# Optimization experiments

Hardware: AMD Instinct MI355X
Metric: run time of the kernel (lower is better)

## Reference

```python
import jax, jax.numpy as jnp
import numpy as np

N_NODES = 50000


def _add_self_loops(edge_index, n):
    loops = jnp.arange(n, dtype=edge_index.dtype)
    src = jnp.concatenate([edge_index[0], loops])
    dst = jnp.concatenate([edge_index[1], loops])
    return src, dst


def _gcn_norm(src, dst, n):
    # symmetric normalization deg^-1/2 (degrees include self-loops), as in PyG GCNConv
    ones = jnp.ones_like(dst, dtype=jnp.float32)
    deg = jax.ops.segment_sum(ones, dst, num_segments=n)
    dinv = jnp.where(deg > 0, jax.lax.rsqrt(deg), 0.0)
    return dinv[src] * dinv[dst]


def _gcn_conv(x, W, b, src, dst, norm, n):
    h = x @ W                                  # [N, d_out] dense transform first (d_out <= d_in)
    msg = h[src] * norm[:, None]               # gather + per-edge scale
    out = jax.ops.segment_sum(msg, dst, num_segments=n)  # scatter-add aggregation
    return out + b


def setup_inputs() -> dict:
    key = jax.random.key(0)
    ks = jax.random.split(key, 5)
    n, e = N_NODES, 1_600_000
    x = jax.random.normal(ks[0], (n, 512), dtype=jnp.float32)
    edge_index = jax.random.randint(ks[1], (2, e), 0, n, dtype=jnp.int64)
    def glorot(k, fi, fo):
        s = jnp.sqrt(6.0 / (fi + fo)).astype(jnp.float32)
        return jax.random.uniform(k, (fi, fo), jnp.float32, -s, s)
    return {
        "x": x,
        "edge_index": edge_index,
        "W0": glorot(ks[2], 512, 256), "b0": jnp.zeros((256,), jnp.float32),
        "W1": glorot(ks[3], 256, 256), "b1": jnp.zeros((256,), jnp.float32),
        "W2": glorot(ks[4], 256, 128), "b2": jnp.zeros((128,), jnp.float32),
    }


def reference(x, edge_index, W0, b0, W1, b1, W2, b2):
    n = x.shape[0]
    src, dst = _add_self_loops(edge_index, n)
    norm = _gcn_norm(src, dst, n)
    h = jax.nn.relu(_gcn_conv(x, W0, b0, src, dst, norm, n))
    h = jax.nn.relu(_gcn_conv(h, W1, b1, src, dst, norm, n))
    z = _gcn_conv(h, W2, b2, src, dst, norm, n)
    return z
```

## Files before the change

### kernel.cpp

```cpp
#include <hip/hip_runtime.h>
#include <hip/hip_bf16.h>
#include <type_traits>

#define NN 50000
#define CNT_S 16

typedef __attribute__((ext_vector_type(8))) short bf16x8;
typedef __attribute__((ext_vector_type(4))) float f32x4;
typedef unsigned int u32;

__device__ __forceinline__ ushort f2bf(float f) {
    unsigned u = __builtin_bit_cast(unsigned, f);
    unsigned r = (u + 0x7fffu + ((u >> 16) & 1u)) >> 16;
    return (ushort)r;
}
__device__ __forceinline__ float bflo(unsigned v) { return __builtin_bit_cast(float, v << 16); }
__device__ __forceinline__ float bfhi(unsigned v) { return __builtin_bit_cast(float, v & 0xffff0000u); }

__device__ __forceinline__ void gld16(const void* g, void* l) {
    __builtin_amdgcn_global_load_lds((const __attribute__((address_space(1))) u32*)g,
                                     (__attribute__((address_space(3))) u32*)l, 16, 0, 0);
}

__global__ void k_initw(int* cnt, int ncnt, const unsigned int* ei, int npairs, int* flag,
                        const float* __restrict__ W0, ushort* __restrict__ WT0,
                        const float* __restrict__ W1, ushort* __restrict__ WT1,
                        const float* __restrict__ W2, ushort* __restrict__ WT2) {
    int id = blockIdx.x * 256 + threadIdx.x;
    if (id < ncnt) cnt[id] = 0;
    if (blockIdx.x == 0) {
        __shared__ int any_nz;
        if (threadIdx.x == 0) any_nz = 0;
        __syncthreads();
        for (int p = threadIdx.x; p < npairs; p += blockDim.x) {
            if (ei[2 * p + 1] != 0u) atomicOr(&any_nz, 1);
        }
        __syncthreads();
        if (threadIdx.x == 0) *flag = (any_nz == 0) ? 1 : 0;
    }
    const float* W; ushort* WT; int K, N, loc;
    if (id < 131072)      { W = W0; WT = WT0; K = 512; N = 256; loc = id; }
    else if (id < 196608) { W = W1; WT = WT1; K = 256; N = 256; loc = id - 131072; }
    else if (id < 229376) { W = W2; WT = WT2; K = 256; N = 128; loc = id - 196608; }
    else return;
    int nn = loc / K, k = loc - nn * K;
    WT[loc] = f2bf(W[(long long)k * N + nn]);
}

__device__ __forceinline__ int load_idx(const void* ei, long long pos, int is64) {
    return is64 ? (int)(((const long long*)ei)[pos]) : ((const int*)ei)[pos];
}

__global__ void k_count(const void* ei, long long E, const int* flag,
                        int* cnt, int* __restrict__ ord) {
    long long e = (long long)blockIdx.x * blockDim.x + threadIdx.x;
    if (e < E) {
        int dst = load_idx(ei, E + e, *flag);
        ord[e] = atomicAdd(&cnt[(long long)dst * CNT_S], 1);
    }
}

__global__ void k_scan(const int* __restrict__ cnt, int* __restrict__ offs,
                       float* __restrict__ dinv, int n) {
    __shared__ int wsum[16];
    __shared__ int carry_s;
    int t = (int)threadIdx.x;
    int lane = t & 63, w = t >> 6;
    if (t == 0) carry_s = 0;
    __syncthreads();
    for (int base = 0; base < n; base += 1024) {
        int i = base + t;
        int v = (i < n) ? cnt[(long long)i * CNT_S] : 0;
        int pv = (v + 7) & ~7;
        int x = pv;
#pragma unroll
        for (int off = 1; off < 64; off <<= 1) {
            int y = __shfl_up(x, off);
            if (lane >= off) x += y;
        }
        if (lane == 63) wsum[w] = x;
        __syncthreads();
        if (w == 0) {
            int pvv = (lane < 16) ? wsum[lane] : 0;
#pragma unroll
            for (int off = 1; off < 16; off <<= 1) {
                int py = __shfl_up(pvv, off);
                if (lane >= off) pvv += py;
            }
            if (lane < 16) wsum[lane] = pvv;
        }
        __syncthreads();
        int wbase = (w > 0) ? wsum[w - 1] : 0;
        int incl = x + wbase;
        int excl = incl - pv;
        int carry = carry_s;
        if (i < n) {
            offs[i] = carry + excl;
            dinv[i] = rsqrtf((float)(v + 1));
        }
        __syncthreads();
        if (t == 1023) carry_s = carry + incl;
        __syncthreads();
    }
    if (threadIdx.x == 0) offs[n] = carry_s;
}

#define KE 8
__global__ void k_bucket(const void* ei, long long E, const int* __restrict__ flag,
                         const float* __restrict__ dinv, const int* __restrict__ offs,
                         const int* __restrict__ ord, int2* __restrict__ epk,
                         const int* __restrict__ cnt, int n, int nchunk_e, int pn) {
    int p = blockIdx.x & 7;
    int c = blockIdx.x >> 3;
    int lo = p * pn;
    int hi = lo + pn; if (hi > n) hi = n;
    if (c < nchunk_e) {
        int is64 = *flag;
        long long base = (long long)c * (256 * KE) + threadIdx.x;
#pragma unroll
        for (int k = 0; k < KE; ++k) {
            long long e = base + k * 256;
            if (e < E) {
                int dst = load_idx(ei, E + e, is64);
                if (dst >= lo && dst < hi) {
                    int src = load_idx(ei, e, is64);
                    int pos = offs[dst] + ord[e];
                    epk[pos] = make_int2(src, __builtin_bit_cast(int, dinv[src] * dinv[dst]));
                }
            }
        }
    } else {
        int i = lo + (c - nchunk_e) * 256 + (int)threadIdx.x;
        if (i < hi) {
            int b = offs[i] + cnt[(long long)i * CNT_S], en = offs[i + 1];
            for (int j = b; j < en; ++j) epk[j] = make_int2(0, 0);
        }
    }
}

__global__ void k_x2bf(const float* __restrict__ x, ushort* __restrict__ xbf, long long n8) {
    long long id = (long long)blockIdx.x * blockDim.x + threadIdx.x;
    if (id < n8) {
        const float* src = x + id * 8;
        float4 f0 = *(const float4*)src;
        float4 f1 = *(const float4*)(src + 4);
        ushort tmp[8] = {f2bf(f0.x), f2bf(f0.y), f2bf(f0.z), f2bf(f0.w),
                         f2bf(f1.x), f2bf(f1.y), f2bf(f1.z), f2bf(f1.w)};
        *(uint4*)&xbf[id * 8] = *(uint4*)tmp;
    }
}

#define LOFF(r, s) (((r) * 8 + ((s) ^ ((r) & 7))) * 8)

template <typename TA>
__global__ __launch_bounds__(256) void k_gemm_mfma(const TA* __restrict__ A,
                                                   const ushort* __restrict__ WT,
                                                   ushort* __restrict__ C,
                                                   int M, int N, int K) {
    __shared__ ushort As[8192];
    __shared__ ushort Bs[8192];
    int t = threadIdx.x;
    int lane = t & 63;
    int w = t >> 6;
    int wr = (w >> 1) * 64, wc = (w & 1) * 64;
    int m0 = blockIdx.y * 128, n0 = blockIdx.x * 128;

    f32x4 acc[4][4] = {};

    for (int k0 = 0; k0 < K; k0 += 64) {
#pragma unroll
        for (int j = 0; j < 4; ++j) {
            int id = (w * 4 + j) * 64 + lane;
            int r = id >> 3, sp = id & 7;
            int s = sp ^ (r & 7);
            gld16(WT + (long long)(n0 + r) * K + k0 + s * 8, &Bs[(r * 8 + sp) * 8]);
        }
        if constexpr (std::is_same<TA, float>::value) {
#pragma unroll
            for (int j = 0; j < 4; ++j) {
                int id = t + j * 256;
                int r = id >> 3, s = id & 7;
                int grow = m0 + r;
                if (grow < M) {
                    const float* src = A + (long long)grow * K + k0 + s * 8;
                    float4 f0 = *(const float4*)src;
                    float4 f1 = *(const float4*)(src + 4);
                    ushort tmp[8] = {f2bf(f0.x), f2bf(f0.y), f2bf(f0.z), f2bf(f0.w),
                                     f2bf(f1.x), f2bf(f1.y), f2bf(f1.z), f2bf(f1.w)};
                    *(uint4*)&As[LOFF(r, s)] = *(uint4*)tmp;
                }
            }
        } else {
#pragma unroll
            for (int j = 0; j < 4; ++j) {
                int rbase = (w * 4 + j) * 8;
                if (m0 + rbase < M) {
                    int id = rbase * 8 + lane;
                    int r = id >> 3, sp = id & 7;
                    int s = sp ^ (r & 7);
                    gld16((const ushort*)A + (long long)(m0 + r) * K + k0 + s * 8,
                          &As[(r * 8 + sp) * 8]);
                }
            }
        }
        __syncthreads();
#pragma unroll
        for (int kk = 0; kk < 2; ++kk) {
            int ks = kk * 4 + (lane >> 4);
            bf16x8 a[4], b[4];
#pragma unroll
            for (int m = 0; m < 4; ++m)
                a[m] = *(bf16x8*)&As[LOFF(wr + m * 16 + (lane & 15), ks)];
#pragma unroll
            for (int nn = 0; nn < 4; ++nn)
                b[nn] = *(bf16x8*)&Bs[LOFF(wc + nn * 16 + (lane & 15), ks)];
#pragma unroll
            for (int m = 0; m < 4; ++m)
#pragma unroll
                for (int nn = 0; nn < 4; ++nn)
                    acc[m][nn] = __builtin_amdgcn_mfma_f32_16x16x32_bf16(a[m], b[nn], acc[m][nn], 0, 0, 0);
        }
        __syncthreads();
    }
#pragma unroll
    for (int m = 0; m < 4; ++m) {
#pragma unroll
        for (int i = 0; i < 4; ++i) {
            int row = m0 + wr + m * 16 + (lane >> 4) * 4 + i;
            if (row < M) {
#pragma unroll
                for (int nn = 0; nn < 4; ++nn) {
                    int col = n0 + wc + nn * 16 + (lane & 15);
                    C[(long long)row * N + col] = f2bf(acc[m][nn][i]);
                }
            }
        }
    }
}

template <int DT, bool RELU, bool OUTF32>
__global__ __launch_bounds__(128) void k_aggs(const ushort* __restrict__ h,
                                              const int* __restrict__ offs,
                                              const int2* __restrict__ epk,
                                              const float* __restrict__ dinv,
                                              const float* __restrict__ bias,
                                              void* __restrict__ outp, int n, int foff) {
    int node = __builtin_amdgcn_readfirstlane((int)(blockIdx.x * 2 + (threadIdx.x >> 6)));
    if (node >= n) return;
    int t = (int)threadIdx.x & 63;
    float di = dinv[node];
    float dii = di * di;

    unsigned v0 = *(const unsigned*)&h[(long long)node * DT + foff + t * 2];
    float2 bs = *(const float2*)&bias[foff + t * 2];
    float a0 = bs.x + dii * bflo(v0);
    float a1 = bs.y + dii * bfhi(v0);

    int s = offs[node], e = offs[node + 1];

    for (int j = s; j < e; j += 8) {
        int2 p[8];
#pragma unroll
        for (int u = 0; u < 8; ++u) p[u] = epk[j + u];
        unsigned v[8];
#pragma unroll
        for (int u = 0; u < 8; ++u)
            v[u] = *(const unsigned*)&h[(long long)p[u].x * DT + foff + t * 2];
#pragma unroll
        for (int u = 0; u < 8; ++u) {
            float wgt = __builtin_bit_cast(float, p[u].y);
            a0 += wgt * bflo(v[u]);
            a1 += wgt * bfhi(v[u]);
        }
    }

    if (RELU) { a0 = fmaxf(a0, 0.f); a1 = fmaxf(a1, 0.f); }
    long long oidx = ((long long)node * DT + foff) / 2 + t;
    if constexpr (OUTF32) {
        ((float2*)outp)[oidx] = make_float2(a0, a1);
    } else {
        unsigned pk = (unsigned)f2bf(a0) | ((unsigned)f2bf(a1) << 16);
        ((unsigned*)outp)[oidx] = pk;
    }
}

extern "C" void kernel_launch(void* const* d_in, const int* in_sizes, int n_in,
                              void* d_out, int out_size, void* d_ws, size_t ws_size,
                              hipStream_t stream) {
    const float* x  = (const float*)d_in[0];
    const void*  ei = d_in[1];
    const float* W0 = (const float*)d_in[2];
    const float* b0 = (const float*)d_in[3];
    const float* W1 = (const float*)d_in[4];
    const float* b1 = (const float*)d_in[5];
    const float* W2 = (const float*)d_in[6];
    const float* b2 = (const float*)d_in[7];
    float* out = (float*)d_out;

    const int n = NN;
    const long long E = (long long)in_sizes[1] / 2;
    const int ncnt = n * CNT_S;

    char* ws = (char*)d_ws;
    int*    cnt  = (int*)(ws);
    int*    offs = (int*)(ws + 3400 * 1024);
    float*  dinv = (float*)(ws + 3700 * 1024);
    int*    flag = (int*)(ws + 3960 * 1024);
    int2*   epk  = (int2*)(ws + 4ll * 1024 * 1024);
    ushort* WT0  = (ushort*)(ws + 20ll * 1024 * 1024);
    ushort* WT1  = (ushort*)(ws + 20ll * 1024 * 1024 + 512 * 1024);
    ushort* WT2  = (ushort*)(ws + 20ll * 1024 * 1024 + 768 * 1024);
    ushort* hA   = (ushort*)(ws + 21ll * 1024 * 1024);
    ushort* hB   = (ushort*)(ws + 47ll * 1024 * 1024);
    ushort* xbf  = (ushort*)(ws + 73ll * 1024 * 1024);
    int*    ord  = (int*)hA;
    const size_t need_xbf = 73ll * 1024 * 1024 + 51200000ll;
    const bool have_xbf = (ws_size >= need_xbf);

    {
        int nb = (ncnt + 255) / 256;
        k_initw<<<nb, 256, 0, stream>>>(cnt, ncnt, (const unsigned int*)ei, 4096, flag,
                                        W0, WT0, W1, WT1, W2, WT2);
    }

    k_count<<<(int)((E + 255) / 256), 256, 0, stream>>>(ei, E, flag, cnt, ord);
    k_scan<<<1, 1024, 0, stream>>>(cnt, offs, dinv, n);
    {
        int nchunk_e = (int)((E + 256 * KE - 1) / (256 * KE));
        int pn = (n + 7) / 8;
        int nchunk_pad = (pn + 255) / 256;
        k_bucket<<<8 * (nchunk_e + nchunk_pad), 256, 0, stream>>>(
            ei, E, flag, dinv, offs, ord, epk, cnt, n, nchunk_e, pn);
    }
    if (have_xbf) {
        long long n8 = (long long)n * 512 / 8;
        k_x2bf<<<(int)((n8 + 255) / 256), 256, 0, stream>>>(x, xbf, n8);
    }

    int mt = (n + 127) / 128;
    int nb2 = (n + 1) / 2;

    if (have_xbf) {
        k_gemm_mfma<ushort><<<dim3(2, mt), 256, 0, stream>>>(xbf, WT0, hA, n, 256, 512);
    } else {
        k_gemm_mfma<float><<<dim3(2, mt), 256, 0, stream>>>(x, WT0, hA, n, 256, 512);
    }
    k_aggs<256, true, false><<<nb2, 128, 0, stream>>>(hA, offs, epk, dinv, b0, hB, n, 0);
    k_aggs<256, true, false><<<nb2, 128, 0, stream>>>(hA, offs, epk, dinv, b0, hB, n, 128);

    k_gemm_mfma<ushort><<<dim3(2, mt), 256, 0, stream>>>(hB, WT1, hA, n, 256, 256);
    k_aggs<256, true, false><<<nb2, 128, 0, stream>>>(hA, offs, epk, dinv, b1, hB, n, 0);
    k_aggs<256, true, false><<<nb2, 128, 0, stream>>>(hA, offs, epk, dinv, b1, hB, n, 128);

    k_gemm_mfma<ushort><<<dim3(1, mt), 256, 0, stream>>>(hB, WT2, hA, n, 128, 256);
    k_aggs<128, false, true><<<nb2, 128, 0, stream>>>(hA, offs, epk, dinv, b2, out, n, 0);
}
```

Before: 515.2 us.

## Replace single-block degree scan with three-phase multi-block scan

The exclusive prefix scan over node degrees used to run in one 1024-thread block that looped serially over all nodes. It is now split into three kernels: per-block reduction (which also writes dinv), a single-wavefront scan of the block sums, and a per-block local scan that adds the block base. This spreads the scan across about 49 blocks instead of one, at the cost of two extra kernel launches and reading the counts twice.

```diff
diff --git a/kernel.cpp b/kernel.cpp
--- a/kernel.cpp
+++ b/kernel.cpp
@@ -60,49 +60,70 @@
     }
 }
 
-__global__ void k_scan(const int* __restrict__ cnt, int* __restrict__ offs,
-                       float* __restrict__ dinv, int n) {
+__global__ __launch_bounds__(1024) void k_scan_a(const int* __restrict__ cnt,
+                                                 int* __restrict__ bsum,
+                                                 float* __restrict__ dinv, int n) {
     __shared__ int wsum[16];
-    __shared__ int carry_s;
-    int t = (int)threadIdx.x;
-    int lane = t & 63, w = t >> 6;
-    if (t == 0) carry_s = 0;
+    int i = blockIdx.x * 1024 + threadIdx.x;
+    int lane = (int)threadIdx.x & 63, w = (int)threadIdx.x >> 6;
+    int v = (i < n) ? cnt[(long long)i * CNT_S] : 0;
+    int pv = (v + 7) & ~7;
+    if (i < n) dinv[i] = rsqrtf((float)(v + 1));
+    int s = pv;
+#pragma unroll
+    for (int off = 1; off < 64; off <<= 1) s += __shfl_xor(s, off);
+    if (lane == 0) wsum[w] = s;
     __syncthreads();
-    for (int base = 0; base < n; base += 1024) {
-        int i = base + t;
-        int v = (i < n) ? cnt[(long long)i * CNT_S] : 0;
-        int pv = (v + 7) & ~7;
-        int x = pv;
-#pragma unroll
-        for (int off = 1; off < 64; off <<= 1) {
-            int y = __shfl_up(x, off);
-            if (lane >= off) x += y;
-        }
-        if (lane == 63) wsum[w] = x;
-        __syncthreads();
-        if (w == 0) {
-            int pvv = (lane < 16) ? wsum[lane] : 0;
-#pragma unroll
-            for (int off = 1; off < 16; off <<= 1) {
-                int py = __shfl_up(pvv, off);
-                if (lane >= off) pvv += py;
-            }
-            if (lane < 16) wsum[lane] = pvv;
-        }
-        __syncthreads();
-        int wbase = (w > 0) ? wsum[w - 1] : 0;
-        int incl = x + wbase;
-        int excl = incl - pv;
-        int carry = carry_s;
-        if (i < n) {
-            offs[i] = carry + excl;
-            dinv[i] = rsqrtf((float)(v + 1));
-        }
-        __syncthreads();
-        if (t == 1023) carry_s = carry + incl;
-        __syncthreads();
-    }
-    if (threadIdx.x == 0) offs[n] = carry_s;
+    if (threadIdx.x == 0) {
+        int t = 0;
+#pragma unroll
+        for (int k = 0; k < 16; ++k) t += wsum[k];
+        bsum[blockIdx.x] = t;
+    }
+}
+
+__global__ void k_scan_b(const int* __restrict__ bsum, int* __restrict__ bbase,
+                         int* __restrict__ offs_n, int nb) {
+    int lane = (int)threadIdx.x;
+    int v = (lane < nb) ? bsum[lane] : 0;
+    int x = v;
+#pragma unroll
+    for (int off = 1; off < 64; off <<= 1) {
+        int y = __shfl_up(x, off);
+        if (lane >= off) x += y;
+    }
+    if (lane < nb) bbase[lane] = x - v;
+    if (lane == nb - 1) *offs_n = x;
+}
+
+__global__ __launch_bounds__(1024) void k_scan_c(const int* __restrict__ cnt,
+                                                 const int* __restrict__ bbase,
+                                                 int* __restrict__ offs, int n) {
+    __shared__ int wsum[16];
+    int i = blockIdx.x * 1024 + threadIdx.x;
+    int lane = (int)threadIdx.x & 63, w = (int)threadIdx.x >> 6;
+    int v = (i < n) ? cnt[(long long)i * CNT_S] : 0;
+    int pv = (v + 7) & ~7;
+    int x = pv;
+#pragma unroll
+    for (int off = 1; off < 64; off <<= 1) {
+        int y = __shfl_up(x, off);
+        if (lane >= off) x += y;
+    }
+    if (lane == 63) wsum[w] = x;
+    __syncthreads();
+    if (w == 0) {
+        int pvv = (lane < 16) ? wsum[lane] : 0;
+#pragma unroll
+        for (int off = 1; off < 16; off <<= 1) {
+            int py = __shfl_up(pvv, off);
+            if (lane >= off) pvv += py;
+        }
+        if (lane < 16) wsum[lane] = pvv;
+    }
+    __syncthreads();
+    int wbase = (w > 0) ? wsum[w - 1] : 0;
+    if (i < n) offs[i] = bbase[blockIdx.x] + wbase + x - pv;
 }
 
 #define KE 8
@@ -300,12 +321,15 @@
     const int n = NN;
     const long long E = (long long)in_sizes[1] / 2;
     const int ncnt = n * CNT_S;
+    const int nbscan = (n + 1023) / 1024;
 
     char* ws = (char*)d_ws;
     int*    cnt  = (int*)(ws);
     int*    offs = (int*)(ws + 3400 * 1024);
     float*  dinv = (float*)(ws + 3700 * 1024);
     int*    flag = (int*)(ws + 3960 * 1024);
+    int*    bsum = (int*)(ws + 3964 * 1024);
+    int*    bbase= (int*)(ws + 3968 * 1024);
     int2*   epk  = (int2*)(ws + 4ll * 1024 * 1024);
     ushort* WT0  = (ushort*)(ws + 20ll * 1024 * 1024);
     ushort* WT1  = (ushort*)(ws + 20ll * 1024 * 1024 + 512 * 1024);
@@ -324,7 +348,9 @@
     }
 
     k_count<<<(int)((E + 255) / 256), 256, 0, stream>>>(ei, E, flag, cnt, ord);
-    k_scan<<<1, 1024, 0, stream>>>(cnt, offs, dinv, n);
+    k_scan_a<<<nbscan, 1024, 0, stream>>>(cnt, bsum, dinv, n);
+    k_scan_b<<<1, 64, 0, stream>>>(bsum, bbase, &offs[n], nbscan);
+    k_scan_c<<<nbscan, 1024, 0, stream>>>(cnt, bbase, offs, n);
     {
         int nchunk_e = (int)((E + 256 * KE - 1) / (256 * KE));
         int pn = (n + 7) / 8;
```

New measurement: 450.8 us. -12.5%, faster.
